# Optimization experiments

Hardware: AMD Instinct MI355X
Metric: run time of the kernel (lower is better)

The kernel has to match this reference:

```python
import jax, jax.numpy as jnp
import numpy as np

BETA = 0.25  # commitment cost (init kwarg)


def setup_inputs() -> dict:
    key = jax.random.key(0)
    k1, k2 = jax.random.split(key)
    B, C, H, W = 8, 256, 64, 64
    K = 8192  # codebook_size
    z = jax.random.normal(k1, (B, C, H, W), dtype=jnp.float32)
    # torch init is uniform(-1/K, 1/K); use same scale
    codebook = jax.random.uniform(k2, (K, C), dtype=jnp.float32,
                                  minval=-1.0 / K, maxval=1.0 / K)
    return {"z": z, "codebook": codebook}


def reference(z, codebook):
    # z: [B, C, H, W] -> [B, H, W, C]
    z_bhwc = jnp.transpose(z, (0, 2, 3, 1))
    D = codebook.shape[1]
    zf = z_bhwc.reshape(-1, D)  # [N, D]
    # squared euclidean distances: ||z||^2 + ||e||^2 - 2 z.e  -> [N, K]
    d = (jnp.sum(zf * zf, axis=1, keepdims=True)
         + jnp.sum(codebook * codebook, axis=1)
         - 2.0 * jnp.einsum('nd,kd->nk', zf, codebook))
    min_encoding_indices = jnp.argmin(d, axis=1)  # [N]
    z_q = codebook[min_encoding_indices].reshape(z_bhwc.shape)  # [B,H,W,C]
    sg = jax.lax.stop_gradient
    # legacy=False branch
    loss = (BETA * jnp.mean((sg(z_q) - z_bhwc) ** 2)
            + jnp.mean((z_q - sg(z_bhwc)) ** 2))
    # straight-through estimator
    z_q = z_bhwc + sg(z_q - z_bhwc)
    z_q = jnp.transpose(z_q, (0, 3, 1, 2))  # back to [B, C, H, W]
    return z_q, loss, min_encoding_indices
```

## Files before the change

### kernel.cpp

```cpp
#include <hip/hip_runtime.h>
#include <hip/hip_bf16.h>
#include <math.h>

typedef unsigned short u16;
typedef unsigned int u32;
typedef unsigned long long u64;
typedef __attribute__((ext_vector_type(8))) _Float16 f16x8;
typedef __attribute__((ext_vector_type(4))) float f32x4;

#define B_   8
#define C_   256
#define HW_  4096
#define N_   32768
#define K_   8192

#define O_LOSSP 0ULL
#define O_E2    16384ULL
#define O_ZN2   49152ULL
#define O_IDX   180224ULL
#define O_ZT    311296ULL
#define O_AP    33865728ULL
#define O_BP    50642944ULL
#define O_CAND  54837248ULL
#define WS_NEED 88391680ULL

#define THRESH_T 9e-5f

__device__ __forceinline__ u16 f2h(float f) {
    _Float16 h = (_Float16)f;
    return __builtin_bit_cast(u16, h);
}

__device__ __forceinline__ void gload16(const void* g, void* l) {
    __builtin_amdgcn_global_load_lds((const __attribute__((address_space(1))) void*)g,
                                     (__attribute__((address_space(3))) void*)l, 16, 0, 0);
}

__global__ __launch_bounds__(256) void vq_prep_z(const float* __restrict__ z,
                                                 float* __restrict__ zT,
                                                 u16* __restrict__ Ap,
                                                 float* __restrict__ zn2g) {
    __shared__ float zl[128][65];
    const int tid = threadIdx.x;
    const int bb = blockIdx.x >> 6;
    const int hwc = blockIdx.x & 63;
    const int hw0 = hwc * 64;
    const int n0 = bb * HW_ + hw0;
    const int lane = tid & 63, wid = tid >> 6;
    const int u = tid & 7;
    double zacc[2] = { 0.0, 0.0 };

    for (int h = 0; h < 2; ++h) {
        __syncthreads();
        for (int c0 = 0; c0 < 128; c0 += 4) {
            int c = c0 + (tid >> 6);
            zl[c][tid & 63] = z[((size_t)(bb * C_ + h * 128 + c)) * HW_ + hw0 + (tid & 63)];
        }
        __syncthreads();
        for (int it = 0; it < 8; ++it) {
            int rp = it * 8 + wid * 2 + (lane >> 5);
            int c4 = (lane & 31) * 4;
            float4 v = { zl[c4][rp], zl[c4 + 1][rp], zl[c4 + 2][rp], zl[c4 + 3][rp] };
            *(float4*)(zT + (size_t)(n0 + rp) * C_ + h * 128 + c4) = v;
        }
        #pragma unroll
        for (int q = 0; q < 2; ++q) {
            const int kc = h * 2 + q;
            #pragma unroll
            for (int rh = 0; rh < 2; ++rh) {
                int rloc = (tid >> 3) + rh * 32;
                int n = n0 + rloc;
                int r = n & 127;
                u16 tmp[8];
                #pragma unroll
                for (int j = 0; j < 8; ++j) {
                    float f = zl[q * 64 + u * 8 + j][rloc];
                    zacc[rh] += (double)f * (double)f;
                    tmp[j] = f2h(f);
                }
                char* dst = (char*)Ap + ((size_t)((n >> 7) * 4 + kc)) * 16384
                          + r * 128 + ((u * 16) ^ ((r & 7) << 4));
                *(uint4*)dst = *(uint4*)tmp;
            }
        }
    }
    #pragma unroll
    for (int rh = 0; rh < 2; ++rh) {
        double a = zacc[rh];
        a += __shfl_xor(a, 1);
        a += __shfl_xor(a, 2);
        a += __shfl_xor(a, 4);
        if (u == 0) zn2g[n0 + (tid >> 3) + rh * 32] = (float)a;
    }
}

__global__ __launch_bounds__(256) void vq_prep_cb(const float* __restrict__ cb,
                                                  u16* __restrict__ Bp,
                                                  float* __restrict__ e2g) {
    const int tid = threadIdx.x;
    const int k0 = blockIdx.x * 64;
    const int u = tid & 7;
    for (int h = 0; h < 2; ++h) {
        int rloc = (tid >> 3) + h * 32;
        int k = k0 + rloc;
        int r = k & 127;
        double eacc = 0.0;
        #pragma unroll
        for (int kc = 0; kc < 4; ++kc) {
            const float* src = cb + (size_t)k * C_ + kc * 64 + u * 8;
            float4 v0 = *(const float4*)(src);
            float4 v1 = *(const float4*)(src + 4);
            float vals[8] = { v0.x, v0.y, v0.z, v0.w, v1.x, v1.y, v1.z, v1.w };
            u16 tmp[8];
            #pragma unroll
            for (int j = 0; j < 8; ++j) {
                eacc += (double)vals[j] * (double)vals[j];
                tmp[j] = f2h(vals[j] * 8192.0f);
            }
            char* dst = (char*)Bp + ((size_t)((k >> 7) * 4 + kc)) * 16384
                      + r * 128 + ((u * 16) ^ ((r & 7) << 4));
            *(uint4*)dst = *(uint4*)tmp;
        }
        eacc += __shfl_xor(eacc, 1);
        eacc += __shfl_xor(eacc, 2);
        eacc += __shfl_xor(eacc, 4);
        if (u == 0) e2g[k] = (float)eacc;
    }
}

__global__ __launch_bounds__(256) void vq_gemm_top2(const u16* __restrict__ Ap,
                                                    const u16* __restrict__ Bp,
                                                    u32* __restrict__ cand) {
    __shared__ char lds[65536];
    const int tid = threadIdx.x;
    const int lane = tid & 63, wid = tid >> 6;
    const int wm = wid >> 1, wn = wid & 1;
    const int l15 = lane & 15, l4 = lane >> 4;

    const int raw = blockIdx.x;
    const int m_tile = raw >> 6;
    const int n_tile = (raw & 7) * 8 + ((raw >> 3) & 7);

    f32x4 acc[4][4];
    #pragma unroll
    for (int i = 0; i < 4; ++i)
        #pragma unroll
        for (int j = 0; j < 4; ++j) acc[i][j] = (f32x4){0.f, 0.f, 0.f, 0.f};

    int rc[4], rz[4], xc[4], xz[4];
    #pragma unroll
    for (int f = 0; f < 4; ++f) {
        rc[f] = wm * 64 + f * 16 + l15;
        rz[f] = wn * 64 + f * 16 + l15;
        xc[f] = (rc[f] & 7) << 4;
        xz[f] = (rz[f] & 7) << 4;
    }
    const int ob = l4 * 16;

    const char* codes_src = (const char*)Bp + (size_t)(n_tile * 4) * 16384;
    const char* z_src     = (const char*)Ap + (size_t)(m_tile * 4) * 16384;

    #define STAGE(buf, kc)                                                        \
        do {                                                                      \
            const char* cs_ = codes_src + (size_t)(kc) * 16384;                   \
            const char* zs_ = z_src + (size_t)(kc) * 16384;                       \
            char* lb_ = lds + (buf) * 32768;                                      \
            _Pragma("unroll")                                                     \
            for (int i_ = 0; i_ < 4; ++i_)                                        \
                gload16(cs_ + i_ * 4096 + tid * 16, lb_ + i_ * 4096 + tid * 16);  \
            _Pragma("unroll")                                                     \
            for (int i_ = 0; i_ < 4; ++i_)                                        \
                gload16(zs_ + i_ * 4096 + tid * 16,                               \
                        lb_ + 16384 + i_ * 4096 + tid * 16);                      \
        } while (0)

    #define COMPUTE(buf)                                                          \
        do {                                                                      \
            const char* base_ = lds + (buf) * 32768;                              \
            _Pragma("unroll")                                                     \
            for (int ks = 0; ks < 2; ++ks) {                                      \
                f16x8 la[4], lb[4];                                               \
                _Pragma("unroll")                                                 \
                for (int f = 0; f < 4; ++f) {                                     \
                    la[f] = *(const f16x8*)(base_ + rc[f] * 128                   \
                                            + ((ks * 64 + ob) ^ xc[f]));          \
                    lb[f] = *(const f16x8*)(base_ + 16384 + rz[f] * 128           \
                                            + ((ks * 64 + ob) ^ xz[f]));          \
                }                                                                 \
                _Pragma("unroll")                                                 \
                for (int fm = 0; fm < 4; ++fm)                                    \
                    _Pragma("unroll")                                             \
                    for (int fn = 0; fn < 4; ++fn)                                \
                        acc[fm][fn] = __builtin_amdgcn_mfma_f32_16x16x32_f16(     \
                            la[fm], lb[fn], acc[fm][fn], 0, 0, 0);                \
            }                                                                     \
        } while (0)

    #define FENCE() __builtin_amdgcn_sched_barrier(0)
    #define WAITB(n)                                                              \
        do {                                                                      \
            asm volatile("s_waitcnt vmcnt(" #n ")" ::: "memory");                 \
            FENCE();                                                              \
            __builtin_amdgcn_s_barrier();                                         \
            FENCE();                                                              \
        } while (0)
    #define ENDBAR()                                                              \
        do {                                                                      \
            __builtin_amdgcn_s_barrier();                                         \
            FENCE();                                                              \
        } while (0)

    STAGE(0, 0);
    STAGE(1, 1);
    WAITB(8);
    COMPUTE(0);
    ENDBAR();
    STAGE(0, 2);
    WAITB(8);
    COMPUTE(1);
    ENDBAR();
    STAGE(1, 3);
    WAITB(8);
    COMPUTE(0);
    WAITB(0);
    COMPUTE(1);

    #undef STAGE
    #undef COMPUTE
    #undef WAITB
    #undef ENDBAR
    #undef FENCE

    const int ktile = n_tile * 2 + wm;
    #pragma unroll
    for (int fn = 0; fn < 4; ++fn) {
        u32 m1 = 0xFFFFFFFFu, m2 = 0xFFFFFFFFu;
        #pragma unroll
        for (int fm = 0; fm < 4; ++fm) {
            #pragma unroll
            for (int rv = 0; rv < 4; ++rv) {
                float w = fmaf(acc[fm][fn][rv], -0x1p-12f, 0.5f);
                u32 p = (__float_as_uint(w) & ~63u) | (u32)(fm * 16 + l4 * 4 + rv);
                u32 t = m1 > p ? m1 : p;
                m1 = m1 < p ? m1 : p;
                m2 = m2 < t ? m2 : t;
            }
        }
        #pragma unroll
        for (int off = 16; off <= 32; off <<= 1) {
            u32 b1 = __shfl_xor(m1, off);
            u32 b2 = __shfl_xor(m2, off);
            u32 t = m1 > b1 ? m1 : b1;
            m1 = m1 < b1 ? m1 : b1;
            u32 s2 = m2 < b2 ? m2 : b2;
            m2 = s2 < t ? s2 : t;
        }
        if (l4 == 0) {
            int rowg = m_tile * 128 + wn * 64 + fn * 16 + l15;
            *(uint2*)(cand + (size_t)rowg * 256 + ktile * 2) = make_uint2(m1, m2);
        }
    }
}

__global__ __launch_bounds__(256) void vq_pick(const u32* __restrict__ cand,
                                               const float* __restrict__ zT,
                                               const float* __restrict__ cb,
                                               const float* __restrict__ e2g,
                                               const float* __restrict__ zn2g,
                                               int* __restrict__ idxg,
                                               float* __restrict__ out) {
    const int lane = threadIdx.x & 63, wid = threadIdx.x >> 6;
    const int row = blockIdx.x * 4 + wid;
    const uint4 e = ((const uint4*)(cand + (size_t)row * 256))[lane];
    u32 m = e.x < e.y ? e.x : e.y;
    u32 mzw = e.z < e.w ? e.z : e.w;
    m = m < mzw ? m : mzw;
    #pragma unroll
    for (int off = 32; off >= 1; off >>= 1) {
        u32 o = __shfl_xor(m, off);
        m = o < m ? o : m;
    }
    const float thr = __uint_as_float(m & ~63u) + THRESH_T;
    const float4 zv = *(const float4*)(zT + (size_t)row * C_ + lane * 4);
    const float zn2a = zn2g[row];
    float bd = INFINITY;
    int bk = 0x7fffffff;
    const u32 ev[4] = { e.x, e.y, e.z, e.w };
    #pragma unroll
    for (int j = 0; j < 4; ++j) {
        u64 msk = __ballot(__uint_as_float(ev[j] & ~63u) <= thr);
        while (msk) {
            const int l = __ffsll((unsigned long long)msk) - 1;
            msk &= msk - 1;
            const u32 val = __shfl(ev[j], l);
            const int k = ((l * 4 + j) >> 1) * 64 + (int)(val & 63u);
            const float4 cv = *(const float4*)(cb + (size_t)k * C_ + lane * 4);
            double s = (double)zv.x * cv.x + (double)zv.y * cv.y
                     + (double)zv.z * cv.z + (double)zv.w * cv.w;
            #pragma unroll
            for (int off = 32; off >= 1; off >>= 1) s += __shfl_xor(s, off);
            const float sf = (float)s;
            const float d = (zn2a + e2g[k]) - 2.0f * sf;
            if (d < bd || (d == bd && k < bk)) { bd = d; bk = k; }
        }
    }
    if (lane == 0) {
        idxg[row] = bk;
        out[8388609 + row] = (float)bk;
    }
}

__global__ __launch_bounds__(256) void vq_zq_loss_kernel(const float* __restrict__ z,
                                                         const float* __restrict__ cb,
                                                         const int* __restrict__ idxg,
                                                         float* __restrict__ out,
                                                         double* __restrict__ partial) {
    double acc = 0.0;
    for (size_t i4 = (size_t)blockIdx.x * 256 + threadIdx.x; i4 < 2097152ULL;
         i4 += 2048ULL * 256ULL) {
        const size_t i = i4 * 4;
        const int hw = (int)(i & 4095);
        const int bc = (int)(i >> 12);
        const int c = bc & 255;
        const int b = bc >> 8;
        const int n = (b << 12) + hw;
        const float4 zv = *(const float4*)(z + i);
        const int k0 = idxg[n], k1 = idxg[n + 1], k2 = idxg[n + 2], k3 = idxg[n + 3];
        const float t0 = cb[(size_t)k0 * C_ + c] - zv.x;
        const float t1 = cb[(size_t)k1 * C_ + c] - zv.y;
        const float t2 = cb[(size_t)k2 * C_ + c] - zv.z;
        const float t3 = cb[(size_t)k3 * C_ + c] - zv.w;
        float4 o = { zv.x + t0, zv.y + t1, zv.z + t2, zv.w + t3 };
        *(float4*)(out + i) = o;
        acc += (double)t0 * t0 + (double)t1 * t1 + (double)t2 * t2 + (double)t3 * t3;
    }
    #pragma unroll
    for (int off = 32; off >= 1; off >>= 1) acc += __shfl_xor(acc, off);
    __shared__ double ls[4];
    const int lane = threadIdx.x & 63, wid = threadIdx.x >> 6;
    if (lane == 0) ls[wid] = acc;
    __syncthreads();
    if (threadIdx.x == 0) partial[blockIdx.x] = ls[0] + ls[1] + ls[2] + ls[3];
}

__global__ __launch_bounds__(256) void vq_loss_final(const double* __restrict__ partial,
                                                     float* __restrict__ out) {
    double acc = 0.0;
    for (int j = threadIdx.x; j < 2048; j += 256) acc += partial[j];
    #pragma unroll
    for (int off = 32; off >= 1; off >>= 1) acc += __shfl_xor(acc, off);
    __shared__ double ls[4];
    const int lane = threadIdx.x & 63, wid = threadIdx.x >> 6;
    if (lane == 0) ls[wid] = acc;
    __syncthreads();
    if (threadIdx.x == 0)
        out[8388608] = (float)(1.25 * (ls[0] + ls[1] + ls[2] + ls[3]) / 8388608.0);
}

__global__ __launch_bounds__(256) void vq_e2_old(const float* __restrict__ cb,
                                                 float* __restrict__ e2g) {
    int lane = threadIdx.x & 63;
    int w = threadIdx.x >> 6;
    int k = blockIdx.x * 4 + w;
    const float4 v = *reinterpret_cast<const float4*>(cb + (size_t)k * C_ + lane * 4);
    double acc = (double)v.x * v.x + (double)v.y * v.y
               + (double)v.z * v.z + (double)v.w * v.w;
    #pragma unroll
    for (int off = 32; off >= 1; off >>= 1) acc += __shfl_xor(acc, off);
    if (lane == 0) e2g[k] = (float)acc;
}

__global__ __launch_bounds__(256) void vq_zn2_old(const float* __restrict__ z,
                                                  float* __restrict__ zn2g) {
    int n = blockIdx.x * 256 + threadIdx.x;
    int b = n >> 12;
    int hw = n & 4095;
    const float* p = z + (size_t)b * C_ * HW_ + hw;
    double acc = 0.0;
    #pragma unroll 8
    for (int c = 0; c < C_; ++c) {
        float v = p[(size_t)c * HW_];
        acc += (double)v * (double)v;
    }
    zn2g[n] = (float)acc;
}

__global__ __launch_bounds__(256) void vq_argmin_old(const float* __restrict__ z,
                                                     const float* __restrict__ cb,
                                                     const float* __restrict__ e2g,
                                                     const float* __restrict__ zn2g,
                                                     int* __restrict__ idxg) {
    __shared__ float zt[C_][32];
    __shared__ float et[64][64];
    const int tid = threadIdx.x;
    const int n0 = blockIdx.x * 32;
    const int b = n0 >> 12;
    const int hw0 = n0 & 4095;
    {
        const int nn = tid & 31;
        const int c8 = tid >> 5;
        #pragma unroll
        for (int j = 0; j < 32; ++j) {
            const int c = j * 8 + c8;
            zt[c][nn] = z[(size_t)(b * C_ + c) * HW_ + hw0 + nn];
        }
    }
    const int cg = tid & 15;
    const int rg = tid >> 4;
    const int r0 = rg * 2;
    __syncthreads();
    const float zn2a = zn2g[n0 + r0];
    const float zn2b = zn2g[n0 + r0 + 1];
    float dmin0 = INFINITY, dmin1 = INFINITY;
    int imin0 = 0, imin1 = 0;
    const int kk = tid >> 2;
    const int c4 = (tid & 3) * 16;
    for (int kt = 0; kt < K_; kt += 64) {
        double s00 = 0, s01 = 0, s02 = 0, s03 = 0;
        double s10 = 0, s11 = 0, s12 = 0, s13 = 0;
        for (int cc = 0; cc < C_; cc += 64) {
            __syncthreads();
            {
                const float* src = cb + (size_t)(kt + kk) * C_ + cc + c4;
                #pragma unroll
                for (int j = 0; j < 16; j += 4) {
                    const float4 v = *reinterpret_cast<const float4*>(src + j);
                    et[c4 + j + 0][kk] = v.x;
                    et[c4 + j + 1][kk] = v.y;
                    et[c4 + j + 2][kk] = v.z;
                    et[c4 + j + 3][kk] = v.w;
                }
            }
            __syncthreads();
            #pragma unroll 4
            for (int c2 = 0; c2 < 64; ++c2) {
                const float2 zv = *reinterpret_cast<const float2*>(&zt[cc + c2][r0]);
                const float4 ev = *reinterpret_cast<const float4*>(&et[c2][cg * 4]);
                const double z0 = (double)zv.x, z1 = (double)zv.y;
                s00 += z0 * ev.x; s01 += z0 * ev.y; s02 += z0 * ev.z; s03 += z0 * ev.w;
                s10 += z1 * ev.x; s11 += z1 * ev.y; s12 += z1 * ev.z; s13 += z1 * ev.w;
            }
        }
        const int kbase = kt + cg * 4;
        const float sf0[4] = {(float)s00, (float)s01, (float)s02, (float)s03};
        const float sf1[4] = {(float)s10, (float)s11, (float)s12, (float)s13};
        #pragma unroll
        for (int j = 0; j < 4; ++j) {
            const int k = kbase + j;
            const float e2k = e2g[k];
            const float d0 = (zn2a + e2k) - 2.0f * sf0[j];
            const float d1 = (zn2b + e2k) - 2.0f * sf1[j];
            if (d0 < dmin0) { dmin0 = d0; imin0 = k; }
            if (d1 < dmin1) { dmin1 = d1; imin1 = k; }
        }
    }
    #pragma unroll
    for (int off = 8; off >= 1; off >>= 1) {
        const float od0 = __shfl_xor(dmin0, off);
        const int   oi0 = __shfl_xor(imin0, off);
        const float od1 = __shfl_xor(dmin1, off);
        const int   oi1 = __shfl_xor(imin1, off);
        if (od0 < dmin0 || (od0 == dmin0 && oi0 < imin0)) { dmin0 = od0; imin0 = oi0; }
        if (od1 < dmin1 || (od1 == dmin1 && oi1 < imin1)) { dmin1 = od1; imin1 = oi1; }
    }
    if (cg == 0) {
        idxg[n0 + r0]     = imin0;
        idxg[n0 + r0 + 1] = imin1;
    }
}

__global__ __launch_bounds__(256) void vq_final_old(const int* __restrict__ idxg,
                                                    float* __restrict__ out) {
    const int i = blockIdx.x * 256 + threadIdx.x;
    out[8388609 + i] = (float)idxg[i];
}

extern "C" void kernel_launch(void* const* d_in, const int* in_sizes, int n_in,
                              void* d_out, int out_size, void* d_ws, size_t ws_size,
                              hipStream_t stream) {
    const float* z  = (const float*)d_in[0];
    const float* cb = (const float*)d_in[1];
    float* out = (float*)d_out;
    char* ws = (char*)d_ws;

    double* lossp = (double*)(ws + O_LOSSP);
    float*  e2g  = (float*)(ws + O_E2);
    float*  zn2g = (float*)(ws + O_ZN2);
    int*    idxg = (int*)(ws + O_IDX);

    if (ws_size >= WS_NEED) {
        float* zT   = (float*)(ws + O_ZT);
        u16*   Ap   = (u16*)(ws + O_AP);
        u16*   Bp   = (u16*)(ws + O_BP);
        u32*   cand = (u32*)(ws + O_CAND);

        hipLaunchKernelGGL(vq_prep_cb, dim3(128), dim3(256), 0, stream, cb, Bp, e2g);
        hipLaunchKernelGGL(vq_prep_z, dim3(512), dim3(256), 0, stream, z, zT, Ap, zn2g);
        hipLaunchKernelGGL(vq_gemm_top2, dim3(16384), dim3(256), 0, stream, Ap, Bp, cand);
        hipLaunchKernelGGL(vq_pick, dim3(N_ / 4), dim3(256), 0, stream,
                           cand, zT, cb, e2g, zn2g, idxg, out);
    } else {
        hipLaunchKernelGGL(vq_e2_old, dim3(K_ / 4), dim3(256), 0, stream, cb, e2g);
        hipLaunchKernelGGL(vq_zn2_old, dim3(N_ / 256), dim3(256), 0, stream, z, zn2g);
        hipLaunchKernelGGL(vq_argmin_old, dim3(N_ / 32), dim3(256), 0, stream,
                           z, cb, e2g, zn2g, idxg);
        hipLaunchKernelGGL(vq_final_old, dim3(N_ / 256), dim3(256), 0, stream, idxg, out);
    }

    hipLaunchKernelGGL(vq_zq_loss_kernel, dim3(2048), dim3(256), 0, stream,
                       z, cb, idxg, out, lossp);
    hipLaunchKernelGGL(vq_loss_final, dim3(1), dim3(256), 0, stream, lossp, out);
}
```

Before: 245.0 us.

## Use 32-wide K chunks with 8-step double buffer and skip rescoring single candidates

```diff
diff --git a/kernel.cpp b/kernel.cpp
--- a/kernel.cpp
+++ b/kernel.cpp
@@ -35,6 +35,7 @@
     __builtin_amdgcn_global_load_lds((const __attribute__((address_space(1))) void*)g,
                                      (__attribute__((address_space(3))) void*)l, 16, 0, 0);
 }
+
 
 __global__ __launch_bounds__(256) void vq_prep_z(const float* __restrict__ z,
                                                  float* __restrict__ zT,
@@ -47,8 +48,11 @@
     const int hw0 = hwc * 64;
     const int n0 = bb * HW_ + hw0;
     const int lane = tid & 63, wid = tid >> 6;
-    const int u = tid & 7;
-    double zacc[2] = { 0.0, 0.0 };
+    const int r = tid >> 2;
+    const int u4 = tid & 3;
+    const int n = n0 + r;
+    const int r7 = n & 127;
+    double zacc = 0.0;
 
     for (int h = 0; h < 2; ++h) {
         __syncthreads();
@@ -64,34 +68,22 @@
             *(float4*)(zT + (size_t)(n0 + rp) * C_ + h * 128 + c4) = v;
         }
         #pragma unroll
-        for (int q = 0; q < 2; ++q) {
-            const int kc = h * 2 + q;
+        for (int q = 0; q < 4; ++q) {
+            u16 tmp[8];
             #pragma unroll
-            for (int rh = 0; rh < 2; ++rh) {
-                int rloc = (tid >> 3) + rh * 32;
-                int n = n0 + rloc;
-                int r = n & 127;
-                u16 tmp[8];
-                #pragma unroll
-                for (int j = 0; j < 8; ++j) {
-                    float f = zl[q * 64 + u * 8 + j][rloc];
-                    zacc[rh] += (double)f * (double)f;
-                    tmp[j] = f2h(f);
-                }
-                char* dst = (char*)Ap + ((size_t)((n >> 7) * 4 + kc)) * 16384
-                          + r * 128 + ((u * 16) ^ ((r & 7) << 4));
-                *(uint4*)dst = *(uint4*)tmp;
+            for (int j = 0; j < 8; ++j) {
+                float f = zl[q * 32 + u4 * 8 + j][r];
+                zacc += (double)f * (double)f;
+                tmp[j] = f2h(f);
             }
-        }
-    }
-    #pragma unroll
-    for (int rh = 0; rh < 2; ++rh) {
-        double a = zacc[rh];
-        a += __shfl_xor(a, 1);
-        a += __shfl_xor(a, 2);
-        a += __shfl_xor(a, 4);
-        if (u == 0) zn2g[n0 + (tid >> 3) + rh * 32] = (float)a;
-    }
+            char* dst = (char*)Ap + ((size_t)((n >> 7) * 8 + h * 4 + q)) * 8192
+                      + r7 * 64 + ((u4 * 16) ^ ((r7 & 3) << 4));
+            *(uint4*)dst = *(uint4*)tmp;
+        }
+    }
+    zacc += __shfl_xor(zacc, 1);
+    zacc += __shfl_xor(zacc, 2);
+    if (u4 == 0) zn2g[n] = (float)zacc;
 }
 
 __global__ __launch_bounds__(256) void vq_prep_cb(const float* __restrict__ cb,
@@ -99,39 +91,36 @@
                                                   float* __restrict__ e2g) {
     const int tid = threadIdx.x;
     const int k0 = blockIdx.x * 64;
-    const int u = tid & 7;
-    for (int h = 0; h < 2; ++h) {
-        int rloc = (tid >> 3) + h * 32;
-        int k = k0 + rloc;
-        int r = k & 127;
-        double eacc = 0.0;
-        #pragma unroll
-        for (int kc = 0; kc < 4; ++kc) {
-            const float* src = cb + (size_t)k * C_ + kc * 64 + u * 8;
-            float4 v0 = *(const float4*)(src);
-            float4 v1 = *(const float4*)(src + 4);
-            float vals[8] = { v0.x, v0.y, v0.z, v0.w, v1.x, v1.y, v1.z, v1.w };
-            u16 tmp[8];
-            #pragma unroll
-            for (int j = 0; j < 8; ++j) {
-                eacc += (double)vals[j] * (double)vals[j];
-                tmp[j] = f2h(vals[j] * 8192.0f);
-            }
-            char* dst = (char*)Bp + ((size_t)((k >> 7) * 4 + kc)) * 16384
-                      + r * 128 + ((u * 16) ^ ((r & 7) << 4));
-            *(uint4*)dst = *(uint4*)tmp;
-        }
-        eacc += __shfl_xor(eacc, 1);
-        eacc += __shfl_xor(eacc, 2);
-        eacc += __shfl_xor(eacc, 4);
-        if (u == 0) e2g[k] = (float)eacc;
-    }
+    const int r = tid >> 2;
+    const int u4 = tid & 3;
+    const int k = k0 + r;
+    const int r7 = k & 127;
+    double eacc = 0.0;
+    #pragma unroll
+    for (int kc8 = 0; kc8 < 8; ++kc8) {
+        const float* src = cb + (size_t)k * C_ + kc8 * 32 + u4 * 8;
+        float4 v0 = *(const float4*)(src);
+        float4 v1 = *(const float4*)(src + 4);
+        float vals[8] = { v0.x, v0.y, v0.z, v0.w, v1.x, v1.y, v1.z, v1.w };
+        u16 tmp[8];
+        #pragma unroll
+        for (int j = 0; j < 8; ++j) {
+            eacc += (double)vals[j] * (double)vals[j];
+            tmp[j] = f2h(vals[j] * 8192.0f);
+        }
+        char* dst = (char*)Bp + ((size_t)((k >> 7) * 8 + kc8)) * 8192
+                  + r7 * 64 + ((u4 * 16) ^ ((r7 & 3) << 4));
+        *(uint4*)dst = *(uint4*)tmp;
+    }
+    eacc += __shfl_xor(eacc, 1);
+    eacc += __shfl_xor(eacc, 2);
+    if (u4 == 0) e2g[k] = (float)eacc;
 }
 
 __global__ __launch_bounds__(256) void vq_gemm_top2(const u16* __restrict__ Ap,
                                                     const u16* __restrict__ Bp,
                                                     u32* __restrict__ cand) {
-    __shared__ char lds[65536];
+    __shared__ char lds[32768];
     const int tid = threadIdx.x;
     const int lane = tid & 63, wid = tid >> 6;
     const int wm = wid >> 1, wn = wid & 1;
@@ -152,84 +141,52 @@
     for (int f = 0; f < 4; ++f) {
         rc[f] = wm * 64 + f * 16 + l15;
         rz[f] = wn * 64 + f * 16 + l15;
-        xc[f] = (rc[f] & 7) << 4;
-        xz[f] = (rz[f] & 7) << 4;
+        xc[f] = (rc[f] & 3) << 4;
+        xz[f] = (rz[f] & 3) << 4;
     }
     const int ob = l4 * 16;
 
-    const char* codes_src = (const char*)Bp + (size_t)(n_tile * 4) * 16384;
-    const char* z_src     = (const char*)Ap + (size_t)(m_tile * 4) * 16384;
+    const char* codes_src = (const char*)Bp + (size_t)n_tile * 65536;
+    const char* z_src     = (const char*)Ap + (size_t)m_tile * 65536;
 
     #define STAGE(buf, kc)                                                        \
         do {                                                                      \
-            const char* cs_ = codes_src + (size_t)(kc) * 16384;                   \
-            const char* zs_ = z_src + (size_t)(kc) * 16384;                       \
-            char* lb_ = lds + (buf) * 32768;                                      \
-            _Pragma("unroll")                                                     \
-            for (int i_ = 0; i_ < 4; ++i_)                                        \
-                gload16(cs_ + i_ * 4096 + tid * 16, lb_ + i_ * 4096 + tid * 16);  \
-            _Pragma("unroll")                                                     \
-            for (int i_ = 0; i_ < 4; ++i_)                                        \
-                gload16(zs_ + i_ * 4096 + tid * 16,                               \
-                        lb_ + 16384 + i_ * 4096 + tid * 16);                      \
+            const char* cs_ = codes_src + (size_t)(kc) * 8192;                    \
+            const char* zs_ = z_src + (size_t)(kc) * 8192;                        \
+            char* lb_ = lds + (buf) * 16384;                                      \
+            gload16(cs_ + tid * 16, lb_ + tid * 16);                              \
+            gload16(cs_ + 4096 + tid * 16, lb_ + 4096 + tid * 16);                \
+            gload16(zs_ + tid * 16, lb_ + 8192 + tid * 16);                       \
+            gload16(zs_ + 4096 + tid * 16, lb_ + 12288 + tid * 16);               \
         } while (0)
 
     #define COMPUTE(buf)                                                          \
         do {                                                                      \
-            const char* base_ = lds + (buf) * 32768;                              \
+            const char* base_ = lds + (buf) * 16384;                              \
+            f16x8 la[4], lb[4];                                                   \
             _Pragma("unroll")                                                     \
-            for (int ks = 0; ks < 2; ++ks) {                                      \
-                f16x8 la[4], lb[4];                                               \
+            for (int f = 0; f < 4; ++f) {                                         \
+                la[f] = *(const f16x8*)(base_ + rc[f] * 64 + (ob ^ xc[f]));       \
+                lb[f] = *(const f16x8*)(base_ + 8192 + rz[f] * 64 + (ob ^ xz[f]));\
+            }                                                                     \
+            _Pragma("unroll")                                                     \
+            for (int fm = 0; fm < 4; ++fm)                                        \
                 _Pragma("unroll")                                                 \
-                for (int f = 0; f < 4; ++f) {                                     \
-                    la[f] = *(const f16x8*)(base_ + rc[f] * 128                   \
-                                            + ((ks * 64 + ob) ^ xc[f]));          \
-                    lb[f] = *(const f16x8*)(base_ + 16384 + rz[f] * 128           \
-                                            + ((ks * 64 + ob) ^ xz[f]));          \
-                }                                                                 \
-                _Pragma("unroll")                                                 \
-                for (int fm = 0; fm < 4; ++fm)                                    \
-                    _Pragma("unroll")                                             \
-                    for (int fn = 0; fn < 4; ++fn)                                \
-                        acc[fm][fn] = __builtin_amdgcn_mfma_f32_16x16x32_f16(     \
-                            la[fm], lb[fn], acc[fm][fn], 0, 0, 0);                \
-            }                                                                     \
+                for (int fn = 0; fn < 4; ++fn)                                    \
+                    acc[fm][fn] = __builtin_amdgcn_mfma_f32_16x16x32_f16(         \
+                        la[fm], lb[fn], acc[fm][fn], 0, 0, 0);                    \
         } while (0)
 
-    #define FENCE() __builtin_amdgcn_sched_barrier(0)
-    #define WAITB(n)                                                              \
-        do {                                                                      \
-            asm volatile("s_waitcnt vmcnt(" #n ")" ::: "memory");                 \
-            FENCE();                                                              \
-            __builtin_amdgcn_s_barrier();                                         \
-            FENCE();                                                              \
-        } while (0)
-    #define ENDBAR()                                                              \
-        do {                                                                      \
-            __builtin_amdgcn_s_barrier();                                         \
-            FENCE();                                                              \
-        } while (0)
-
     STAGE(0, 0);
-    STAGE(1, 1);
-    WAITB(8);
-    COMPUTE(0);
-    ENDBAR();
-    STAGE(0, 2);
-    WAITB(8);
-    COMPUTE(1);
-    ENDBAR();
-    STAGE(1, 3);
-    WAITB(8);
-    COMPUTE(0);
-    WAITB(0);
-    COMPUTE(1);
+    #pragma unroll
+    for (int kc = 0; kc < 8; ++kc) {
+        __syncthreads();
+        if (kc < 7) STAGE((kc + 1) & 1, kc + 1);
+        COMPUTE(kc & 1);
+    }
 
     #undef STAGE
     #undef COMPUTE
-    #undef WAITB
-    #undef ENDBAR
-    #undef FENCE
 
     const int ktile = n_tile * 2 + wm;
     #pragma unroll
@@ -281,27 +238,42 @@
         m = o < m ? o : m;
     }
     const float thr = __uint_as_float(m & ~63u) + THRESH_T;
-    const float4 zv = *(const float4*)(zT + (size_t)row * C_ + lane * 4);
-    const float zn2a = zn2g[row];
-    float bd = INFINITY;
-    int bk = 0x7fffffff;
     const u32 ev[4] = { e.x, e.y, e.z, e.w };
+    u64 msk[4];
+    int tot = 0;
     #pragma unroll
     for (int j = 0; j < 4; ++j) {
-        u64 msk = __ballot(__uint_as_float(ev[j] & ~63u) <= thr);
-        while (msk) {
-            const int l = __ffsll((unsigned long long)msk) - 1;
-            msk &= msk - 1;
-            const u32 val = __shfl(ev[j], l);
-            const int k = ((l * 4 + j) >> 1) * 64 + (int)(val & 63u);
-            const float4 cv = *(const float4*)(cb + (size_t)k * C_ + lane * 4);
-            double s = (double)zv.x * cv.x + (double)zv.y * cv.y
-                     + (double)zv.z * cv.z + (double)zv.w * cv.w;
-            #pragma unroll
-            for (int off = 32; off >= 1; off >>= 1) s += __shfl_xor(s, off);
-            const float sf = (float)s;
-            const float d = (zn2a + e2g[k]) - 2.0f * sf;
-            if (d < bd || (d == bd && k < bk)) { bd = d; bk = k; }
+        msk[j] = __ballot(__uint_as_float(ev[j] & ~63u) <= thr);
+        tot += __popcll((unsigned long long)msk[j]);
+    }
+    int bk;
+    if (tot == 1) {
+        const int j = msk[0] ? 0 : (msk[1] ? 1 : (msk[2] ? 2 : 3));
+        const int l = __ffsll((unsigned long long)msk[j]) - 1;
+        const u32 val = __shfl(ev[j], l);
+        bk = ((l * 4 + j) >> 1) * 64 + (int)(val & 63u);
+    } else {
+        const float4 zv = *(const float4*)(zT + (size_t)row * C_ + lane * 4);
+        const float zn2a = zn2g[row];
+        float bd = INFINITY;
+        bk = 0x7fffffff;
+        #pragma unroll
+        for (int j = 0; j < 4; ++j) {
+            u64 mj = msk[j];
+            while (mj) {
+                const int l = __ffsll((unsigned long long)mj) - 1;
+                mj &= mj - 1;
+                const u32 val = __shfl(ev[j], l);
+                const int k = ((l * 4 + j) >> 1) * 64 + (int)(val & 63u);
+                const float4 cv = *(const float4*)(cb + (size_t)k * C_ + lane * 4);
+                double s = (double)zv.x * cv.x + (double)zv.y * cv.y
+                         + (double)zv.z * cv.z + (double)zv.w * cv.w;
+                #pragma unroll
+                for (int off = 32; off >= 1; off >>= 1) s += __shfl_xor(s, off);
+                const float sf = (float)s;
+                const float d = (zn2a + e2g[k]) - 2.0f * sf;
+                if (d < bd || (d == bd && k < bk)) { bd = d; bk = k; }
+            }
         }
     }
     if (lane == 0) {
```

Result: faster. 227.2 us (-7.3%).
